# Kernel optimization log

Hardware: AMD Instinct MI355X
Metric: run time of the kernel (lower is better)

The kernel has to match this reference:

```python
import jax, jax.numpy as jnp
import numpy as np

R, N, F, H, C = 3, 100000, 256, 128, 2
N0, S1, D1, S2, D2 = 16384, 16384, 4096, 4096, 512


def setup_inputs() -> dict:
    key = jax.random.key(0)
    ks = jax.random.split(key, 13)
    return {
        "features": jax.random.normal(ks[0], (N, F), jnp.float32),
        "src_nodes": jax.random.randint(ks[1], (R, N0), 0, N),
        "dstsrc2src1": jax.random.randint(ks[2], (R, S1), 0, N0),
        "dstsrc2dst1": jax.random.randint(ks[3], (R, D1), 0, N0),
        "dif_mat1": jax.random.uniform(ks[4], (R, D1, S1), jnp.float32) / S1,
        "dstsrc2src2": jax.random.randint(ks[5], (R, S2), 0, D1),
        "dstsrc2dst2": jax.random.randint(ks[6], (R, D2), 0, D1),
        "dif_mat2": jax.random.uniform(ks[7], (R, D2, S2), jnp.float32) / S2,
        "w1": jax.random.normal(ks[8], (2 * F, H), jnp.float32) * 0.05,
        "w2": jax.random.normal(ks[9], (2 * H, H), jnp.float32) * 0.05,
        "relation_vectors": jax.random.uniform(ks[10], (R, H), jnp.float32),
        "attention_vec": jax.random.uniform(ks[11], (2 * H, 1), jnp.float32),
        "classifier_w": jax.random.normal(ks[12], (H, C), jnp.float32) * 0.05,
    }


def _agg(x, d2s, d2d, dif, w, rel_vec, att_vec):
    # x: [n, din]; dif: [d, s]; w: [2*din, H]
    agg = dif @ x[d2s]                                  # mean-diffused neighbor feats [d, din]
    h = jnp.concatenate([agg, x[d2d]], axis=1) @ w      # [d, H]
    rel = jnp.broadcast_to(rel_vec[None, :], (h.shape[0], rel_vec.shape[0]))
    score = (jnp.concatenate([h, rel], axis=1) @ att_vec)[:, 0]  # [d]
    att = jax.nn.softmax(score)                         # softmax over batch nodes
    return h * att[:, None]


def reference(features, src_nodes, dstsrc2src1, dstsrc2dst1, dif_mat1,
              dstsrc2src2, dstsrc2dst2, dif_mat2, w1, w2,
              relation_vectors, attention_vec, classifier_w):
    def per_relation(src, s1, d1, m1, s2, d2, m2, rel_vec):
        x = features[src]                               # gather node feats [N0, F]
        x = _agg(x, s1, d1, m1, w1, rel_vec, attention_vec)   # [D1, H]
        x = _agg(x, s2, d2, m2, w2, rel_vec, attention_vec)   # [D2, H]
        return x

    xs = jax.vmap(per_relation)(src_nodes, dstsrc2src1, dstsrc2dst1, dif_mat1,
                                dstsrc2src2, dstsrc2dst2, dif_mat2, relation_vectors)
    summed = jnp.sum(xs, axis=0)                        # sum over relations [D2, H]
    inv_norm = jax.lax.rsqrt(jnp.maximum(jnp.sum(summed * summed, axis=1, keepdims=True), 1e-12))
    normed = summed * inv_norm                          # tf.nn.l2_normalize(axis=1)
    return jax.nn.softmax(normed @ classifier_w, axis=-1)
```

## Files before the change

### kernel.cpp

```cpp
#include <hip/hip_runtime.h>
#include <hip/hip_bf16.h>
#include <math.h>

constexpr int Rc  = 3;
constexpr int Fc  = 256;
constexpr int Hc  = 128;
constexpr int N0c = 16384;
constexpr int S1c = 16384;
constexpr int D1c = 4096;
constexpr int S2c = 4096;
constexpr int D2c = 512;
constexpr int KH1 = 4;
constexpr int KH2 = 16;

typedef __bf16 bf16x8 __attribute__((ext_vector_type(8)));
typedef float  f32x4  __attribute__((ext_vector_type(4)));

__device__ __forceinline__ void glds16(const void* g, void* l) {
  __builtin_amdgcn_global_load_lds(
      (const __attribute__((address_space(1))) void*)g,
      (__attribute__((address_space(3))) void*)l, 16, 0, 0);
}

__device__ __forceinline__ bf16x8 cvt2(const float4 a, const float4 b) {
  bf16x8 c;
  c[0] = (__bf16)a.x; c[1] = (__bf16)a.y; c[2] = (__bf16)a.z; c[3] = (__bf16)a.w;
  c[4] = (__bf16)b.x; c[5] = (__bf16)b.y; c[6] = (__bf16)b.z; c[7] = (__bf16)b.w;
  return c;
}

__device__ __forceinline__ unsigned short bfbits(float v) {
  __bf16 b = (__bf16)v; unsigned short u;
  __builtin_memcpy(&u, &b, 2); return u;
}

__global__ __launch_bounds__(256, 2)
void wpack(const float* __restrict__ w1, const float* __restrict__ w2,
           unsigned char* __restrict__ wp, float* __restrict__ esum) {
  const int tile = blockIdx.x, half = blockIdx.y, t = threadIdx.x;
  if (tile == 0 && half == 0 && t < 8) esum[t] = 0.f;
  const float* src; int row0;
  if (tile < 4)       { src = w1; row0 = tile * 64; }
  else if (tile < 8)  { src = w1; row0 = 256 + (tile - 4) * 64; }
  else if (tile < 10) { src = w2; row0 = (tile - 8) * 64; }
  else                { src = w2; row0 = 128 + (tile - 10) * 64; }
  unsigned char* dst = wp + ((size_t)half * 12 + tile) * 16384;
  __shared__ float sm[64][132];
  {
    const int r = t >> 2, c0 = (t & 3) * 32;
#pragma unroll
    for (int j = 0; j < 8; j++)
      *(float4*)&sm[r][c0 + 4 * j] = *(const float4*)(src + (size_t)(row0 + r) * 128 + c0 + 4 * j);
  }
  __syncthreads();
  if (t < 128) {
    const int n = t;
#pragma unroll
    for (int ch = 0; ch < 8; ch++) {
      bf16x8 o;
#pragma unroll
      for (int e = 0; e < 8; e++) {
        float v = sm[ch * 8 + e][n];
        __bf16 h = (__bf16)v;
        o[e] = half ? (__bf16)(v - (float)h) : h;
      }
      *(bf16x8*)(dst + n * 128 + ((ch ^ (n & 7)) * 16)) = o;
    }
  }
}

__global__ __launch_bounds__(256, 3)
void gg0(const float* __restrict__ feat, const int* __restrict__ srcn,
         const int* __restrict__ d2s1, const unsigned char* __restrict__ wp,
         unsigned char* __restrict__ xgwp) {
  const int rel = blockIdx.y, bx = blockIdx.x, s0 = bx * 64;
  const unsigned char* Bh = wp;
  const unsigned char* Bl = wp + (size_t)12 * 16384;

  const int t = threadIdx.x, lane = t & 63, w = t >> 6;
  const int mh = w >> 1, nh = w & 1;

  __shared__ __bf16 Asm[64 * 64];
  __shared__ __bf16 Bhs[128 * 64];
  __shared__ __bf16 Bls[128 * 64];

  const int arow = t >> 2, ak0 = (t & 3) * 16;
  const int row = s0 + arow;
  const size_t arowg = (size_t)srcn[rel * N0c + d2s1[(size_t)rel * S1c + row]];
  const float* aptr = feat + arowg * Fc + ak0;
  const int ac0 = ak0 >> 3;
  __bf16* asw0 = &Asm[arow * 64 + ((ac0    ) ^ (arow & 7)) * 8];
  __bf16* asw1 = &Asm[arow * 64 + ((ac0 + 1) ^ (arow & 7)) * 8];

  float4 a[16];
#pragma unroll
  for (int tl = 0; tl < 4; tl++)
#pragma unroll
    for (int j = 0; j < 4; j++) a[tl * 4 + j] = *(const float4*)(aptr + tl * 64 + 4 * j);

  f32x4 acc[2][4] = {};

  for (int tl = 0; tl < 4; ++tl) {
    asm volatile("s_waitcnt lgkmcnt(0)" ::: "memory");
    __builtin_amdgcn_s_barrier();
    __builtin_amdgcn_sched_barrier(0);
    {
      const unsigned char* bh = Bh + (size_t)tl * 16384 + w * 4096 + lane * 16;
      const unsigned char* bl = Bl + (size_t)tl * 16384 + w * 4096 + lane * 16;
      char* dh = (char*)Bhs + w * 4096;
      char* dl = (char*)Bls + w * 4096;
#pragma unroll
      for (int i = 0; i < 4; i++) glds16(bh + i * 1024, dh + i * 1024);
#pragma unroll
      for (int i = 0; i < 4; i++) glds16(bl + i * 1024, dl + i * 1024);
    }
    *(bf16x8*)asw0 = cvt2(a[tl * 4 + 0], a[tl * 4 + 1]);
    *(bf16x8*)asw1 = cvt2(a[tl * 4 + 2], a[tl * 4 + 3]);
    asm volatile("s_waitcnt vmcnt(0) lgkmcnt(0)" ::: "memory");
    __builtin_amdgcn_s_barrier();
    __builtin_amdgcn_sched_barrier(0);
#pragma unroll
    for (int ks = 0; ks < 2; ks++) {
      const int ch = ks * 4 + (lane >> 4);
      bf16x8 af[2], bh[4], bl[4];
#pragma unroll
      for (int mi = 0; mi < 2; mi++) {
        int r = mh * 32 + mi * 16 + (lane & 15);
        af[mi] = *(const bf16x8*)&Asm[r * 64 + ((ch ^ (r & 7)) * 8)];
      }
#pragma unroll
      for (int ni = 0; ni < 4; ni++) {
        int n = nh * 64 + ni * 16 + (lane & 15);
        bh[ni] = *(const bf16x8*)&Bhs[n * 64 + ((ch ^ (n & 7)) * 8)];
        bl[ni] = *(const bf16x8*)&Bls[n * 64 + ((ch ^ (n & 7)) * 8)];
      }
#pragma unroll
      for (int mi = 0; mi < 2; mi++)
#pragma unroll
        for (int ni = 0; ni < 4; ni++) {
          acc[mi][ni] = __builtin_amdgcn_mfma_f32_16x16x32_bf16(af[mi], bh[ni], acc[mi][ni], 0, 0, 0);
          acc[mi][ni] = __builtin_amdgcn_mfma_f32_16x16x32_bf16(af[mi], bl[ni], acc[mi][ni], 0, 0, 0);
        }
    }
  }
  unsigned char* tile = xgwp + ((size_t)(rel * (S1c >> 6) + bx)) * 16384;
#pragma unroll
  for (int mi = 0; mi < 2; mi++)
#pragma unroll
    for (int ni = 0; ni < 4; ni++) {
      const int sl0 = mh * 32 + mi * 16 + (lane >> 4) * 4;
      const int n = nh * 64 + ni * 16 + (lane & 15);
      const int ch = sl0 >> 3, e0 = sl0 & 7, cs = ch ^ (n & 7);
      ushort4 u;
      u.x = bfbits(acc[mi][ni][0]); u.y = bfbits(acc[mi][ni][1]);
      u.z = bfbits(acc[mi][ni][2]); u.w = bfbits(acc[mi][ni][3]);
      *(ushort4*)(tile + n * 128 + cs * 16 + e0 * 2) = u;
    }
}

__global__ __launch_bounds__(256, 3)
void big1p(const float* __restrict__ dif1, const unsigned char* __restrict__ xgwp,
           float* __restrict__ aggP, const float* __restrict__ feat,
           const int* __restrict__ srcn, const int* __restrict__ d2d1,
           const unsigned char* __restrict__ wp, float* __restrict__ xdw) {
  __shared__ char lds[40960];
  const int t = threadIdx.x, lane = t & 63, w = t >> 6;
  const int mh = w >> 1, nh = w & 1;

  if (blockIdx.x < 768) {
    __bf16* Asm  = (__bf16*)lds;
    __bf16* Bsm0 = (__bf16*)(lds + 8192);
    __bf16* Bsm1 = (__bf16*)(lds + 24576);
    const int F = blockIdx.x;
    const int xcd = F & 7, r = F >> 3;
    const int sub = r >> 5, m = r & 31;
    const int h = xcd + 8 * sub;
    const int g = h >> 1;
    const int rel = g >> 2, kh = g & 3;
    const int m0 = ((h & 1) * 32 + m) * 64;
    constexpr int NT = 64;

    const float* Ag = dif1 + ((size_t)rel * D1c + m0) * S1c + (size_t)kh * 4096;
    const unsigned char* Bt = xgwp + ((size_t)rel * 256 + (size_t)kh * NT) * 16384;
    float* Cg = aggP + (((size_t)kh * Rc + rel) * D1c + m0) * 128;

    f32x4 acc[2][4] = {};
    const int arow = t >> 2, ak0 = (t & 3) * 16;
    const float* aptr = Ag + (size_t)arow * S1c + ak0;
    const int ac0 = ak0 >> 3;
    __bf16* asw0 = &Asm[arow * 64 + ((ac0    ) ^ (arow & 7)) * 8];
    __bf16* asw1 = &Asm[arow * 64 + ((ac0 + 1) ^ (arow & 7)) * 8];
    const unsigned char* bsrc = Bt + w * 4096 + lane * 16;

    float4 a0[4], a1[4], a2[4];
    {
      char* bd = (char*)Bsm0 + w * 4096;
#pragma unroll
      for (int i = 0; i < 4; i++) glds16(bsrc + i * 1024, bd + i * 1024);
    }
#pragma unroll
    for (int j = 0; j < 4; j++) a0[j] = *(const float4*)(aptr + 4 * j);
#pragma unroll
    for (int j = 0; j < 4; j++) a1[j] = *(const float4*)(aptr + 64 + 4 * j);

    for (int tl = 0; tl < NT; ++tl) {
      __bf16* Bc = (tl & 1) ? Bsm1 : Bsm0;
      __bf16* Bn = (tl & 1) ? Bsm0 : Bsm1;
      asm volatile("s_waitcnt lgkmcnt(0)" ::: "memory");
      __builtin_amdgcn_s_barrier();
      __builtin_amdgcn_sched_barrier(0);
      if (tl + 1 < NT) {
        const unsigned char* bs = bsrc + (size_t)(tl + 1) * 16384;
        char* bd = (char*)Bn + w * 4096;
#pragma unroll
        for (int i = 0; i < 4; i++) glds16(bs + i * 1024, bd + i * 1024);
      }
      if (tl + 2 < NT) {
        const float* ap = aptr + (size_t)(tl + 2) * 64;
#pragma unroll
        for (int j = 0; j < 4; j++) a2[j] = *(const float4*)(ap + 4 * j);
      }
      *(bf16x8*)asw0 = cvt2(a0[0], a0[1]);
      *(bf16x8*)asw1 = cvt2(a0[2], a0[3]);
      if (tl + 2 < NT)
        asm volatile("s_waitcnt vmcnt(12) lgkmcnt(0)" ::: "memory");
      else if (tl + 1 < NT)
        asm volatile("s_waitcnt vmcnt(8) lgkmcnt(0)" ::: "memory");
      else
        asm volatile("s_waitcnt vmcnt(0) lgkmcnt(0)" ::: "memory");
      __builtin_amdgcn_s_barrier();
      __builtin_amdgcn_sched_barrier(0);
#pragma unroll
      for (int ks = 0; ks < 2; ks++) {
        const int ch = ks * 4 + (lane >> 4);
        bf16x8 af[2], bfr[4];
#pragma unroll
        for (int mi = 0; mi < 2; mi++) {
          int rr = mh * 32 + mi * 16 + (lane & 15);
          af[mi] = *(const bf16x8*)&Asm[rr * 64 + ((ch ^ (rr & 7)) * 8)];
        }
#pragma unroll
        for (int ni = 0; ni < 4; ni++) {
          int n = nh * 64 + ni * 16 + (lane & 15);
          bfr[ni] = *(const bf16x8*)&Bc[n * 64 + ((ch ^ (n & 7)) * 8)];
        }
#pragma unroll
        for (int mi = 0; mi < 2; mi++)
#pragma unroll
          for (int ni = 0; ni < 4; ni++)
            acc[mi][ni] = __builtin_amdgcn_mfma_f32_16x16x32_bf16(af[mi], bfr[ni], acc[mi][ni], 0, 0, 0);
      }
#pragma unroll
      for (int j = 0; j < 4; j++) { a0[j] = a1[j]; a1[j] = a2[j]; }
    }
#pragma unroll
    for (int mi = 0; mi < 2; mi++)
#pragma unroll
      for (int ni = 0; ni < 4; ni++) {
        const int col = nh * 64 + ni * 16 + (lane & 15);
#pragma unroll
        for (int j = 0; j < 4; j++) {
          const int rr = mh * 32 + mi * 16 + (lane >> 4) * 4 + j;
          Cg[(size_t)rr * 128 + col] = acc[mi][ni][j];
        }
      }
  } else {
    __bf16* Asm = (__bf16*)lds;
    __bf16* Bhs = (__bf16*)(lds + 8192);
    __bf16* Bls = (__bf16*)(lds + 24576);
    const int jb = blockIdx.x - 768;
    const int rel = jb >> 6, bx = jb & 63, s0 = bx * 64;
    const unsigned char* Bh = wp + (size_t)4 * 16384;
    const unsigned char* Bl = wp + (size_t)16 * 16384;

    const int arow = t >> 2, ak0 = (t & 3) * 16;
    const int row = s0 + arow;
    const size_t arowg = (size_t)srcn[rel * N0c + d2d1[(size_t)rel * D1c + row]];
    const float* aptr = feat + arowg * Fc + ak0;
    const int ac0 = ak0 >> 3;
    __bf16* asw0 = &Asm[arow * 64 + ((ac0    ) ^ (arow & 7)) * 8];
    __bf16* asw1 = &Asm[arow * 64 + ((ac0 + 1) ^ (arow & 7)) * 8];

    float4 a[16];
#pragma unroll
    for (int tl = 0; tl < 4; tl++)
#pragma unroll
      for (int j = 0; j < 4; j++) a[tl * 4 + j] = *(const float4*)(aptr + tl * 64 + 4 * j);

    f32x4 acc[2][4] = {};
    for (int tl = 0; tl < 4; ++tl) {
      asm volatile("s_waitcnt lgkmcnt(0)" ::: "memory");
      __builtin_amdgcn_s_barrier();
      __builtin_amdgcn_sched_barrier(0);
      {
        const unsigned char* bh = Bh + (size_t)tl * 16384 + w * 4096 + lane * 16;
        const unsigned char* bl = Bl + (size_t)tl * 16384 + w * 4096 + lane * 16;
        char* dh = (char*)Bhs + w * 4096;
        char* dl = (char*)Bls + w * 4096;
#pragma unroll
        for (int i = 0; i < 4; i++) glds16(bh + i * 1024, dh + i * 1024);
#pragma unroll
        for (int i = 0; i < 4; i++) glds16(bl + i * 1024, dl + i * 1024);
      }
      *(bf16x8*)asw0 = cvt2(a[tl * 4 + 0], a[tl * 4 + 1]);
      *(bf16x8*)asw1 = cvt2(a[tl * 4 + 2], a[tl * 4 + 3]);
      asm volatile("s_waitcnt vmcnt(0) lgkmcnt(0)" ::: "memory");
      __builtin_amdgcn_s_barrier();
      __builtin_amdgcn_sched_barrier(0);
#pragma unroll
      for (int ks = 0; ks < 2; ks++) {
        const int ch = ks * 4 + (lane >> 4);
        bf16x8 af[2], bh[4], bl[4];
#pragma unroll
        for (int mi = 0; mi < 2; mi++) {
          int r = mh * 32 + mi * 16 + (lane & 15);
          af[mi] = *(const bf16x8*)&Asm[r * 64 + ((ch ^ (r & 7)) * 8)];
        }
#pragma unroll
        for (int ni = 0; ni < 4; ni++) {
          int n = nh * 64 + ni * 16 + (lane & 15);
          bh[ni] = *(const bf16x8*)&Bhs[n * 64 + ((ch ^ (n & 7)) * 8)];
          bl[ni] = *(const bf16x8*)&Bls[n * 64 + ((ch ^ (n & 7)) * 8)];
        }
#pragma unroll
        for (int mi = 0; mi < 2; mi++)
#pragma unroll
          for (int ni = 0; ni < 4; ni++) {
            acc[mi][ni] = __builtin_amdgcn_mfma_f32_16x16x32_bf16(af[mi], bh[ni], acc[mi][ni], 0, 0, 0);
            acc[mi][ni] = __builtin_amdgcn_mfma_f32_16x16x32_bf16(af[mi], bl[ni], acc[mi][ni], 0, 0, 0);
          }
      }
    }
#pragma unroll
    for (int mi = 0; mi < 2; mi++)
#pragma unroll
      for (int ni = 0; ni < 4; ni++) {
        const int col = nh * 64 + ni * 16 + (lane & 15);
#pragma unroll
        for (int j = 0; j < 4; j++) {
          const int rr = mh * 32 + mi * 16 + (lane >> 4) * 4 + j;
          xdw[((size_t)rel * D1c + s0 + rr) * 128 + col] = acc[mi][ni][j];
        }
      }
  }
}

__global__ __launch_bounds__(256, 3)
void gemm_big(const float* __restrict__ A, const unsigned char* __restrict__ Bp,
              float* __restrict__ C, int M, int KTOT, int KH) {
  const int rel = blockIdx.z, kh = blockIdx.y, m0 = blockIdx.x * 64;
  const int t = threadIdx.x, lane = t & 63, w = t >> 6;
  const int KB = KTOT / KH, NT = KB >> 6;
  const int mh = w >> 1, nh = w & 1;

  const float* Ag = A + ((size_t)rel * M + m0) * KTOT + (size_t)kh * KB;
  const unsigned char* Bt = Bp + ((size_t)rel * (KTOT >> 6) + (size_t)kh * NT) * 16384;
  float* Cg = C + (((size_t)kh * Rc + rel) * M + m0) * 128;

  __shared__ __bf16 Asm[64 * 64];
  __shared__ __bf16 Bsm[2][128 * 64];

  f32x4 acc[2][4] = {};
  const int arow = t >> 2, ak0 = (t & 3) * 16;
  const float* aptr = Ag + (size_t)arow * KTOT + ak0;
  const int ac0 = ak0 >> 3;
  __bf16* asw0 = &Asm[arow * 64 + ((ac0    ) ^ (arow & 7)) * 8];
  __bf16* asw1 = &Asm[arow * 64 + ((ac0 + 1) ^ (arow & 7)) * 8];
  const unsigned char* bsrc = Bt + w * 4096 + lane * 16;

  float4 a0[4], a1[4];
#pragma unroll
  for (int j = 0; j < 4; j++) a0[j] = *(const float4*)(aptr + 4 * j);
  {
    char* bd = (char*)Bsm[0] + w * 4096;
#pragma unroll
    for (int i = 0; i < 4; i++) glds16(bsrc + i * 1024, bd + i * 1024);
  }

  for (int tl = 0; tl < NT; ++tl) {
    const int cur = tl & 1;
    asm volatile("s_waitcnt lgkmcnt(0)" ::: "memory");
    __builtin_amdgcn_s_barrier();
    __builtin_amdgcn_sched_barrier(0);
    if (tl + 1 < NT) {
      const unsigned char* bs = bsrc + (size_t)(tl + 1) * 16384;
      char* bd = (char*)Bsm[cur ^ 1] + w * 4096;
#pragma unroll
      for (int i = 0; i < 4; i++) glds16(bs + i * 1024, bd + i * 1024);
      const float* ap = aptr + (size_t)(tl + 1) * 64;
#pragma unroll
      for (int j = 0; j < 4; j++) a1[j] = *(const float4*)(ap + 4 * j);
    }
    *(bf16x8*)asw0 = cvt2(a0[0], a0[1]);
    *(bf16x8*)asw1 = cvt2(a0[2], a0[3]);
    if (tl + 1 < NT)
      asm volatile("s_waitcnt vmcnt(8) lgkmcnt(0)" ::: "memory");
    else
      asm volatile("s_waitcnt vmcnt(0) lgkmcnt(0)" ::: "memory");
    __builtin_amdgcn_s_barrier();
    __builtin_amdgcn_sched_barrier(0);
    const __bf16* Bc = Bsm[cur];
#pragma unroll
    for (int ks = 0; ks < 2; ks++) {
      const int ch = ks * 4 + (lane >> 4);
      bf16x8 af[2], bfr[4];
#pragma unroll
      for (int mi = 0; mi < 2; mi++) {
        int r = mh * 32 + mi * 16 + (lane & 15);
        af[mi] = *(const bf16x8*)&Asm[r * 64 + ((ch ^ (r & 7)) * 8)];
      }
#pragma unroll
      for (int ni = 0; ni < 4; ni++) {
        int n = nh * 64 + ni * 16 + (lane & 15);
        bfr[ni] = *(const bf16x8*)&Bc[n * 64 + ((ch ^ (n & 7)) * 8)];
      }
#pragma unroll
      for (int mi = 0; mi < 2; mi++)
#pragma unroll
        for (int ni = 0; ni < 4; ni++)
          acc[mi][ni] = __builtin_amdgcn_mfma_f32_16x16x32_bf16(af[mi], bfr[ni], acc[mi][ni], 0, 0, 0);
    }
#pragma unroll
    for (int j = 0; j < 4; j++) a0[j] = a1[j];
  }
#pragma unroll
  for (int mi = 0; mi < 2; mi++)
#pragma unroll
    for (int ni = 0; ni < 4; ni++) {
      const int col = nh * 64 + ni * 16 + (lane & 15);
#pragma unroll
      for (int j = 0; j < 4; j++) {
        const int r = mh * 32 + mi * 16 + (lane >> 4) * 4 + j;
        Cg[(size_t)r * 128 + col] = acc[mi][ni][j];
      }
    }
}

__global__ __launch_bounds__(256, 3)
void c1_l2(const float* __restrict__ aggP, const float* __restrict__ xdw,
           const float* __restrict__ attv, const unsigned char* __restrict__ wp,
           float* __restrict__ escore1, float* __restrict__ esum,
           float* __restrict__ P, float* __restrict__ Q) {
  const int rel = blockIdx.y, d0 = blockIdx.x * 64;
  const int t = threadIdx.x, lane = t & 63, w = t >> 6;
  const int mh = w >> 1, nh = w & 1;

  __shared__ __bf16 Asm[64 * 128];
  __shared__ __bf16 Bhs[128 * 64];
  __shared__ __bf16 Bls[128 * 64];
  __shared__ float  sred[64];

  const int r = t >> 2, c0 = (t & 3) * 32;
  float4 x0[8];
  {
    const size_t base = ((size_t)rel * D1c + d0 + r) * 128 + c0;
#pragma unroll
    for (int j = 0; j < 8; j++) x0[j] = *(const float4*)(xdw + base + 4 * j);
#pragma unroll
    for (int p2 = 0; p2 < KH1; p2++) {
      const float* ap = aggP + (((size_t)p2 * Rc + rel) * D1c + d0 + r) * 128 + c0;
#pragma unroll
      for (int j = 0; j < 8; j++) {
        float4 u = *(const float4*)(ap + 4 * j);
        x0[j].x += u.x; x0[j].y += u.y; x0[j].z += u.z; x0[j].w += u.w;
      }
    }
  }
  float sp = 0.f;
#pragma unroll
  for (int j = 0; j < 8; j++) {
    sp += x0[j].x * attv[c0 + 4 * j]     + x0[j].y * attv[c0 + 4 * j + 1]
        + x0[j].z * attv[c0 + 4 * j + 2] + x0[j].w * attv[c0 + 4 * j + 3];
  }
  sp += __shfl_xor(sp, 1); sp += __shfl_xor(sp, 2);
  const float e = expf(sp);
  if ((t & 3) == 0) { escore1[(size_t)rel * D1c + d0 + r] = e; sred[r] = e; }
  const int ch0 = (t & 3) * 4;
#pragma unroll
  for (int q = 0; q < 4; q++) {
    *(bf16x8*)&Asm[r * 128 + (((ch0 + q) ^ (r & 7)) * 8)] = cvt2(x0[2 * q], x0[2 * q + 1]);
  }
  __syncthreads();
  if (t < 64) {
    float v = sred[t];
    v += __shfl_down(v, 32); v += __shfl_down(v, 16); v += __shfl_down(v, 8);
    v += __shfl_down(v, 4);  v += __shfl_down(v, 2);  v += __shfl_down(v, 1);
    if (t == 0) atomicAdd(esum + rel, v);
  }
  f32x4 accP[2][4] = {}, accQ[2][4] = {};
#pragma unroll
  for (int z = 0; z < 2; z++) {
#pragma unroll
    for (int tl = 0; tl < 2; tl++) {
      if (!(z == 0 && tl == 0)) {
        asm volatile("s_waitcnt lgkmcnt(0)" ::: "memory");
        __builtin_amdgcn_s_barrier();
        __builtin_amdgcn_sched_barrier(0);
      }
      {
        const unsigned char* bh = wp + (size_t)(8 + z * 2 + tl) * 16384 + w * 4096 + lane * 16;
        const unsigned char* bl = wp + (size_t)(20 + z * 2 + tl) * 16384 + w * 4096 + lane * 16;
        char* dh = (char*)Bhs + w * 4096;
        char* dl = (char*)Bls + w * 4096;
#pragma unroll
        for (int i = 0; i < 4; i++) glds16(bh + i * 1024, dh + i * 1024);
#pragma unroll
        for (int i = 0; i < 4; i++) glds16(bl + i * 1024, dl + i * 1024);
      }
      asm volatile("s_waitcnt vmcnt(0) lgkmcnt(0)" ::: "memory");
      __builtin_amdgcn_s_barrier();
      __builtin_amdgcn_sched_barrier(0);
      f32x4 (*acc)[4] = z ? accQ : accP;
#pragma unroll
      for (int ks = 0; ks < 2; ks++) {
        const int lch = ks * 4 + (lane >> 4);
        const int ch  = tl * 8 + lch;
        bf16x8 af[2], bh[4], bl[4];
#pragma unroll
        for (int mi = 0; mi < 2; mi++) {
          int rr = mh * 32 + mi * 16 + (lane & 15);
          af[mi] = *(const bf16x8*)&Asm[rr * 128 + ((ch ^ (rr & 7)) * 8)];
        }
#pragma unroll
        for (int ni = 0; ni < 4; ni++) {
          int n = nh * 64 + ni * 16 + (lane & 15);
          bh[ni] = *(const bf16x8*)&Bhs[n * 64 + ((lch ^ (n & 7)) * 8)];
          bl[ni] = *(const bf16x8*)&Bls[n * 64 + ((lch ^ (n & 7)) * 8)];
        }
#pragma unroll
        for (int mi = 0; mi < 2; mi++)
#pragma unroll
          for (int ni = 0; ni < 4; ni++) {
            acc[mi][ni] = __builtin_amdgcn_mfma_f32_16x16x32_bf16(af[mi], bh[ni], acc[mi][ni], 0, 0, 0);
            acc[mi][ni] = __builtin_amdgcn_mfma_f32_16x16x32_bf16(af[mi], bl[ni], acc[mi][ni], 0, 0, 0);
          }
      }
    }
  }
#pragma unroll
  for (int mi = 0; mi < 2; mi++)
#pragma unroll
    for (int ni = 0; ni < 4; ni++) {
      const int col = nh * 64 + ni * 16 + (lane & 15);
#pragma unroll
      for (int j = 0; j < 4; j++) {
        const int rr = mh * 32 + mi * 16 + (lane >> 4) * 4 + j;
        P[((size_t)rel * D1c + d0 + rr) * 128 + col] = accP[mi][ni][j];
        Q[((size_t)rel * D1c + d0 + rr) * 128 + col] = accQ[mi][ni][j];
      }
    }
}

__global__ __launch_bounds__(256, 2)
void pgpack(const float* __restrict__ P, const int* __restrict__ d2s2,
            const float* __restrict__ escore1, const float* __restrict__ esum,
            unsigned char* __restrict__ PGp) {
  const int rel = blockIdx.y, kb = blockIdx.x, t = threadIdx.x;
  const float inv1 = 1.0f / esum[rel];
  __shared__ __bf16 sm[64][136];
  {
    const int kl = t >> 2, c0 = (t & 3) * 32;
    const int sr = d2s2[rel * S2c + kb * 64 + kl];
    const float sc = escore1[(size_t)rel * D1c + sr] * inv1;
    const float4* p = (const float4*)(P + ((size_t)rel * D1c + sr) * 128 + c0);
#pragma unroll
    for (int j = 0; j < 4; j++) {
      float4 v0 = p[2 * j], v1 = p[2 * j + 1];
      v0.x *= sc; v0.y *= sc; v0.z *= sc; v0.w *= sc;
      v1.x *= sc; v1.y *= sc; v1.z *= sc; v1.w *= sc;
      *(bf16x8*)&sm[kl][c0 + 8 * j] = cvt2(v0, v1);
    }
  }
  __syncthreads();
  if (t < 128) {
    const int n = t;
    unsigned char* dst = PGp + ((size_t)(rel * (S2c >> 6) + kb)) * 16384;
#pragma unroll
    for (int ch = 0; ch < 8; ch++) {
      bf16x8 o;
#pragma unroll
      for (int e = 0; e < 8; e++) o[e] = sm[ch * 8 + e][n];
      *(bf16x8*)(dst + n * 128 + ((ch ^ (n & 7)) * 16)) = o;
    }
  }
}

__global__ __launch_bounds__(128, 4)
void combine2(const float* __restrict__ aggP2, const float* __restrict__ Q,
              const int* __restrict__ d2d2, const float* __restrict__ attv,
              const float* __restrict__ escore1, const float* __restrict__ esum,
              float* __restrict__ h2, float* __restrict__ escore2) {
  const int rel = blockIdx.y, d0 = blockIdx.x * 8, t = threadIdx.x;
  const float inv1 = 1.0f / esum[rel];
  float acc[8];
#pragma unroll
  for (int i = 0; i < 8; i++) {
    const int d = d0 + i;
    const int qr = d2d2[rel * D2c + d];
    const float qs = escore1[(size_t)rel * D1c + qr] * inv1;
    float v = Q[((size_t)rel * D1c + qr) * 128 + t] * qs;
#pragma unroll
    for (int p = 0; p < KH2; p++)
      v += aggP2[(((size_t)p * Rc + rel) * D2c + d) * 128 + t];
    acc[i] = v;
    h2[((size_t)rel * D2c + d) * 128 + t] = v;
  }
  const float avt = attv[t];
  __shared__ float sred[2][8];
#pragma unroll
  for (int i = 0; i < 8; i++) {
    float p = acc[i] * avt;
    p += __shfl_down(p, 32); p += __shfl_down(p, 16); p += __shfl_down(p, 8);
    p += __shfl_down(p, 4);  p += __shfl_down(p, 2);  p += __shfl_down(p, 1);
    if ((t & 63) == 0) sred[t >> 6][i] = p;
  }
  __syncthreads();
  if (t < 8) {
    const float e2 = expf(sred[0][t] + sred[1][t]);
    escore2[rel * D2c + d0 + t] = e2;
    float v = e2;
    v += __shfl_down(v, 4); v += __shfl_down(v, 2); v += __shfl_down(v, 1);
    if (t == 0) atomicAdd((float*)esum + 4 + rel, v);
  }
}

__global__ __launch_bounds__(128, 4)
void k9_final(const float* __restrict__ h2, const float* __restrict__ escore2,
              const float* __restrict__ esum, const float* __restrict__ cw,
              float* __restrict__ out) {
  const int d = blockIdx.x, t = threadIdx.x;
  float v = 0.f;
#pragma unroll
  for (int r = 0; r < Rc; r++) {
    const float att = escore2[r * D2c + d] / esum[4 + r];
    v += h2[((size_t)r * D2c + d) * Hc + t] * att;
  }
  float ss = v * v;
  ss += __shfl_down(ss, 32); ss += __shfl_down(ss, 16); ss += __shfl_down(ss, 8);
  ss += __shfl_down(ss, 4);  ss += __shfl_down(ss, 2);  ss += __shfl_down(ss, 1);
  __shared__ float sr[3][2];
  if ((t & 63) == 0) sr[0][t >> 6] = ss;
  __syncthreads();
  const float tot = sr[0][0] + sr[0][1];
  const float inv = rsqrtf(fmaxf(tot, 1e-12f));
  const float nv = v * inv;
  float p0 = nv * cw[t * 2], p1 = nv * cw[t * 2 + 1];
  p0 += __shfl_down(p0, 32); p0 += __shfl_down(p0, 16); p0 += __shfl_down(p0, 8);
  p0 += __shfl_down(p0, 4);  p0 += __shfl_down(p0, 2);  p0 += __shfl_down(p0, 1);
  p1 += __shfl_down(p1, 32); p1 += __shfl_down(p1, 16); p1 += __shfl_down(p1, 8);
  p1 += __shfl_down(p1, 4);  p1 += __shfl_down(p1, 2);  p1 += __shfl_down(p1, 1);
  if ((t & 63) == 0) { sr[1][t >> 6] = p0; sr[2][t >> 6] = p1; }
  __syncthreads();
  if (t == 0) {
    const float l0 = sr[1][0] + sr[1][1];
    const float l1 = sr[2][0] + sr[2][1];
    const float m = fmaxf(l0, l1);
    const float e0 = expf(l0 - m), e1 = expf(l1 - m);
    const float is = 1.0f / (e0 + e1);
    out[d * 2 + 0] = e0 * is;
    out[d * 2 + 1] = e1 * is;
  }
}

extern "C" void kernel_launch(void* const* d_in, const int* in_sizes, int n_in,
                              void* d_out, int out_size, void* d_ws, size_t ws_size,
                              hipStream_t stream) {
  (void)in_sizes; (void)n_in; (void)out_size; (void)ws_size;
  const float* feat = (const float*)d_in[0];
  const int*   srcn = (const int*)d_in[1];
  const int*   d2s1 = (const int*)d_in[2];
  const int*   d2d1 = (const int*)d_in[3];
  const float* dif1 = (const float*)d_in[4];
  const int*   d2s2 = (const int*)d_in[5];
  const int*   d2d2 = (const int*)d_in[6];
  const float* dif2 = (const float*)d_in[7];
  const float* w1   = (const float*)d_in[8];
  const float* w2   = (const float*)d_in[9];
  const float* attv = (const float*)d_in[11];
  const float* cw   = (const float*)d_in[12];
  float* out = (float*)d_out;

  char* p = (char*)d_ws;
  auto take = [&](size_t n) { char* r = p; p += (n + 255) & ~(size_t)255; return r; };
  unsigned char* wp   = (unsigned char*)take(24 * 16384);
  unsigned char* xgwp = (unsigned char*)take((size_t)Rc * 256 * 16384);
  float* xdw    = (float*)take((size_t)Rc * D1c * 128 * 4);
  float* aggP   = (float*)take((size_t)KH1 * Rc * D1c * 128 * 4);
  float* escore1= (float*)take((size_t)Rc * D1c * 4);
  float* esum   = (float*)take(256);
  unsigned char* PGp = (unsigned char*)take((size_t)Rc * 64 * 16384);
  float* h2     = (float*)take((size_t)Rc * D2c * 128 * 4);
  float* escore2= (float*)take((size_t)Rc * D2c * 4);
  float* P = (float*)xgwp;
  float* Q = P + (size_t)Rc * D1c * 128;
  float* aggP2 = aggP;

  wpack<<<dim3(12, 2), 256, 0, stream>>>(w1, w2, wp, esum);
  gg0<<<dim3(256, Rc), 256, 0, stream>>>(feat, srcn, d2s1, wp, xgwp);
  big1p<<<960, 256, 0, stream>>>(dif1, xgwp, aggP, feat, srcn, d2d1, wp, xdw);
  c1_l2<<<dim3(D1c / 64, Rc), 256, 0, stream>>>(aggP, xdw, attv, wp, escore1, esum, P, Q);
  pgpack<<<dim3(S2c / 64, Rc), 256, 0, stream>>>(P, d2s2, escore1, esum, PGp);
  gemm_big<<<dim3(D2c / 64, KH2, Rc), 256, 0, stream>>>(dif2, PGp, aggP2, D2c, S2c, KH2);
  combine2<<<dim3(D2c / 8, Rc), 128, 0, stream>>>(aggP2, Q, d2d2, attv, escore1, esum, h2, escore2);
  k9_final<<<D2c, 128, 0, stream>>>(h2, escore2, esum, cw, out);
}
```

Baseline: 286.0 us.

## Restructure dif1 A-tile loads into coalesced 128-float row segments with double-buffered LDS

The fp32 diffusion-matrix tile loader in the big1p GEMM is reorganized so each wave loads 128 contiguous floats per row (half a wave per row, 8 rows per lane), covering two k-steps per load. Those values are converted to bf16 and written into double-buffered A tiles in LDS, with B also double-buffered in a single enlarged LDS region. The goal is wider, more coalesced global reads of the large dif1 matrix and fewer load issues per k-step. In exchange the block uses more LDS (48KB), which may reduce occupancy, and it relies on more complex vmcnt wait accounting.

```diff
diff --git a/kernel.cpp b/kernel.cpp
--- a/kernel.cpp
+++ b/kernel.cpp
@@ -14,6 +14,7 @@
 constexpr int KH2 = 16;
 
 typedef __bf16 bf16x8 __attribute__((ext_vector_type(8)));
+typedef __bf16 bf16x4 __attribute__((ext_vector_type(4)));
 typedef float  f32x4  __attribute__((ext_vector_type(4)));
 
 __device__ __forceinline__ void glds16(const void* g, void* l) {
@@ -163,86 +164,108 @@
            float* __restrict__ aggP, const float* __restrict__ feat,
            const int* __restrict__ srcn, const int* __restrict__ d2d1,
            const unsigned char* __restrict__ wp, float* __restrict__ xdw) {
-  __shared__ char lds[40960];
+  __shared__ char lds[49152];
   const int t = threadIdx.x, lane = t & 63, w = t >> 6;
   const int mh = w >> 1, nh = w & 1;
 
   if (blockIdx.x < 768) {
-    __bf16* Asm  = (__bf16*)lds;
-    __bf16* Bsm0 = (__bf16*)(lds + 8192);
-    __bf16* Bsm1 = (__bf16*)(lds + 24576);
+    __bf16* Abuf = (__bf16*)lds;
+    __bf16* Bbuf = (__bf16*)(lds + 16384);
     const int F = blockIdx.x;
     const int xcd = F & 7, r = F >> 3;
     const int sub = r >> 5, m = r & 31;
     const int h = xcd + 8 * sub;
-    const int g = h >> 1;
-    const int rel = g >> 2, kh = g & 3;
+    const int g2 = h >> 1;
+    const int rel = g2 >> 2, kh = g2 & 3;
     const int m0 = ((h & 1) * 32 + m) * 64;
-    constexpr int NT = 64;
-
-    const float* Ag = dif1 + ((size_t)rel * D1c + m0) * S1c + (size_t)kh * 4096;
-    const unsigned char* Bt = xgwp + ((size_t)rel * 256 + (size_t)kh * NT) * 16384;
+    constexpr int NP = 64;
+    constexpr int NM = 32;
+
+    const unsigned char* Bt = xgwp + ((size_t)rel * 256 + (size_t)kh * NP) * 16384;
     float* Cg = aggP + (((size_t)kh * Rc + rel) * D1c + m0) * 128;
 
+    const int lst = (lane & 31) >> 4;
+    const int lr2 = lane >> 5;
+    const int fo  = (lane & 31) * 4;
+    const int ch  = (fo & 63) >> 3;
+    const int eo  = fo & 7;
+    const float* aW = dif1 + ((size_t)(rel * D1c + m0 + w * 16 + lr2)) * S1c
+                    + (size_t)kh * 4096 + fo;
+    const unsigned char* bsrc = Bt + w * 4096 + lane * 16;
+
     f32x4 acc[2][4] = {};
-    const int arow = t >> 2, ak0 = (t & 3) * 16;
-    const float* aptr = Ag + (size_t)arow * S1c + ak0;
-    const int ac0 = ak0 >> 3;
-    __bf16* asw0 = &Asm[arow * 64 + ((ac0    ) ^ (arow & 7)) * 8];
-    __bf16* asw1 = &Asm[arow * 64 + ((ac0 + 1) ^ (arow & 7)) * 8];
-    const unsigned char* bsrc = Bt + w * 4096 + lane * 16;
-
-    float4 a0[4], a1[4], a2[4];
+    float4 a0[8], a1[8];
+
+#define LOAD_A(ARR, M_) do { _Pragma("unroll") \
+    for (int ri = 0; ri < 8; ri++) \
+      ARR[ri] = *(const float4*)(aW + (size_t)ri * 2 * S1c + (size_t)(M_) * 128); \
+  } while (0)
+
+#define WRITE_A(ARR, NBUF) do { if (lst == (NBUF)) { _Pragma("unroll") \
+    for (int ri = 0; ri < 8; ri++) { \
+      const int row_ = w * 16 + ri * 2 + lr2; \
+      bf16x4 cv_; \
+      cv_[0] = (__bf16)ARR[ri].x; cv_[1] = (__bf16)ARR[ri].y; \
+      cv_[2] = (__bf16)ARR[ri].z; cv_[3] = (__bf16)ARR[ri].w; \
+      *(bf16x4*)&Abuf[(NBUF) * 4096 + row_ * 64 + ((ch ^ (row_ & 7)) * 8) + eo] = cv_; \
+    } } } while (0)
+
+    LOAD_A(a0, 0);
     {
-      char* bd = (char*)Bsm0 + w * 4096;
+      char* bd = (char*)Bbuf + w * 4096;
 #pragma unroll
       for (int i = 0; i < 4; i++) glds16(bsrc + i * 1024, bd + i * 1024);
     }
-#pragma unroll
-    for (int j = 0; j < 4; j++) a0[j] = *(const float4*)(aptr + 4 * j);
-#pragma unroll
-    for (int j = 0; j < 4; j++) a1[j] = *(const float4*)(aptr + 64 + 4 * j);
-
-    for (int tl = 0; tl < NT; ++tl) {
-      __bf16* Bc = (tl & 1) ? Bsm1 : Bsm0;
-      __bf16* Bn = (tl & 1) ? Bsm0 : Bsm1;
+    WRITE_A(a0, 0);
+    LOAD_A(a1, 1);
+
+#pragma unroll 1
+    for (int g = 0; g < NP; ++g) {
+      const int buf = g & 1, nbuf = buf ^ 1;
       asm volatile("s_waitcnt lgkmcnt(0)" ::: "memory");
       __builtin_amdgcn_s_barrier();
       __builtin_amdgcn_sched_barrier(0);
-      if (tl + 1 < NT) {
-        const unsigned char* bs = bsrc + (size_t)(tl + 1) * 16384;
-        char* bd = (char*)Bn + w * 4096;
+      if (g + 1 < NP) {
+        const unsigned char* bs = bsrc + (size_t)(g + 1) * 16384;
+        char* bd = (char*)Bbuf + nbuf * 16384 + w * 4096;
 #pragma unroll
         for (int i = 0; i < 4; i++) glds16(bs + i * 1024, bd + i * 1024);
       }
-      if (tl + 2 < NT) {
-        const float* ap = aptr + (size_t)(tl + 2) * 64;
-#pragma unroll
-        for (int j = 0; j < 4; j++) a2[j] = *(const float4*)(ap + 4 * j);
-      }
-      *(bf16x8*)asw0 = cvt2(a0[0], a0[1]);
-      *(bf16x8*)asw1 = cvt2(a0[2], a0[3]);
-      if (tl + 2 < NT)
+      if (g + 1 < NP) {
+        const int mw = (g + 1) >> 1;
+        if ((mw & 1) == 0) { WRITE_A(a0, nbuf); }
+        else               { WRITE_A(a1, nbuf); }
+      }
+      if (g & 1) {
+        const int mn = (g + 3) >> 1;
+        if (mn < NM) {
+          if ((mn & 1) == 0) { LOAD_A(a0, mn); }
+          else               { LOAD_A(a1, mn); }
+        }
+      }
+      if (g < NP - 2)
         asm volatile("s_waitcnt vmcnt(12) lgkmcnt(0)" ::: "memory");
-      else if (tl + 1 < NT)
-        asm volatile("s_waitcnt vmcnt(8) lgkmcnt(0)" ::: "memory");
+      else if (g == NP - 2)
+        asm volatile("s_waitcnt vmcnt(4) lgkmcnt(0)" ::: "memory");
       else
         asm volatile("s_waitcnt vmcnt(0) lgkmcnt(0)" ::: "memory");
       __builtin_amdgcn_s_barrier();
       __builtin_amdgcn_sched_barrier(0);
+      const __bf16* Ac = Abuf + buf * 4096;
+      const __bf16* Bc = Bbuf + buf * 8192;
 #pragma unroll
       for (int ks = 0; ks < 2; ks++) {
-        const int ch = ks * 4 + (lane >> 4);
+        const int cch = ks * 4 + (lane >> 4);
         bf16x8 af[2], bfr[4];
 #pragma unroll
         for (int mi = 0; mi < 2; mi++) {
           int rr = mh * 32 + mi * 16 + (lane & 15);
-          af[mi] = *(const bf16x8*)&Asm[rr * 64 + ((ch ^ (rr & 7)) * 8)];
+          af[mi] = *(const bf16x8*)&Ac[rr * 64 + ((cch ^ (rr & 7)) * 8)];
         }
 #pragma unroll
         for (int ni = 0; ni < 4; ni++) {
           int n = nh * 64 + ni * 16 + (lane & 15);
-          bfr[ni] = *(const bf16x8*)&Bc[n * 64 + ((ch ^ (n & 7)) * 8)];
+          bfr[ni] = *(const bf16x8*)&Bc[n * 64 + ((cch ^ (n & 7)) * 8)];
         }
 #pragma unroll
         for (int mi = 0; mi < 2; mi++)
@@ -250,9 +273,9 @@
           for (int ni = 0; ni < 4; ni++)
             acc[mi][ni] = __builtin_amdgcn_mfma_f32_16x16x32_bf16(af[mi], bfr[ni], acc[mi][ni], 0, 0, 0);
       }
-#pragma unroll
-      for (int j = 0; j < 4; j++) { a0[j] = a1[j]; a1[j] = a2[j]; }
-    }
+    }
+#undef LOAD_A
+#undef WRITE_A
 #pragma unroll
     for (int mi = 0; mi < 2; mi++)
 #pragma unroll
```

Result: faster. 274.3 us (-4.1%).
